# Optimization experiments

Hardware: AMD Instinct MI355X
Metric: run time of the kernel (lower is better)

The kernel has to match this reference:

```python
import jax, jax.numpy as jnp
import numpy as np

MAX_ITER = 3          # module init arg max_iter
FILL = 1e9            # large finite value for out-of-grid / out-of-label-range padding

N, H, W, C = 1, 320, 640, 32
NUM_DIR = 4


def setup_inputs() -> dict:
    key = jax.random.key(0)
    k1, k2, k3 = jax.random.split(key, 3)
    prob_vol = jax.random.uniform(k1, (N, H, W, C), dtype=jnp.float32)
    edge_weights = jax.random.uniform(k2, (N, NUM_DIR, H, W), dtype=jnp.float32)
    # affinities[:, :, :2] ~ L1 jump costs, affinities[:, :, 2] ~ L2 truncation cost
    affinities = jax.random.uniform(k3, (N, NUM_DIR, 3, H, W), dtype=jnp.float32)
    offset = jnp.zeros((N, NUM_DIR, H, W), dtype=jnp.float32)
    messages = jnp.zeros((N, NUM_DIR, H, W, C), dtype=jnp.float32)
    return {"prob_vol": prob_vol, "edge_weights": edge_weights,
            "affinities": affinities, "offset": offset, "messages": messages}


def _shift(x, axis, step):
    # result[p] = x[p - step] along `axis`, FILL outside the grid
    n = x.shape[axis]
    pw = [(0, 0)] * x.ndim
    if step > 0:
        pw[axis] = (step, 0)
        return jax.lax.slice_in_dim(jnp.pad(x, pw, constant_values=FILL), 0, n, axis=axis)
    pw[axis] = (0, -step)
    return jax.lax.slice_in_dim(jnp.pad(x, pw, constant_values=FILL), -step, n - step, axis=axis)


def _bp_iter(cost, edge, aff, offset, messages):
    # cost: (N,H,W,C); messages: (N,4,H,W,C); edge/offset: (N,4,H,W); aff: (N,4,3,H,W)
    total = cost + messages.sum(axis=1)  # belief pre-message, (N,H,W,C)
    # direction d: (d, opposite, spatial axis, step of sender->receiver)
    DIRS = [(0, 1, 2, 1), (1, 0, 2, -1), (2, 3, 1, 1), (3, 2, 1, -1)]
    new = []
    for d, opp, axis, step in DIRS:
        h = total - messages[:, opp]          # exclude reverse-direction message at sender
        hs = _shift(h, axis, step)            # sender's h aligned to receiver pixel
        w = edge[:, d][..., None]             # (N,H,W,1) edge weight
        if d % 2 == 0:
            a_m1 = aff[:, d, 0][..., None]    # cost for label jump -1
            a_p1 = aff[:, d, 1][..., None]    # cost for label jump +1
        else:  # opposite direction swaps the asymmetric +/-1 jump costs
            a_m1 = aff[:, d, 1][..., None]
            a_p1 = aff[:, d, 0][..., None]
        L2 = aff[:, d, 2][..., None]          # truncation cost for |jump| >= 2
        off = offset[:, d][..., None]
        big = jnp.full(hs.shape[:-1] + (1,), FILL, hs.dtype)
        h_lm1 = jnp.concatenate([big, hs[..., :-1]], axis=-1)  # hs(l-1)
        h_lp1 = jnp.concatenate([hs[..., 1:], big], axis=-1)   # hs(l+1)
        hmin = hs.min(axis=-1, keepdims=True)
        # min-sum update with truncated-linear pairwise: min over jump 0, +-1, truncated
        m = jnp.minimum(jnp.minimum(hs, h_lm1 + w * a_p1),
                        jnp.minimum(h_lp1 + w * a_m1, hmin + w * L2)) + w * off
        m = m - m.min(axis=-1, keepdims=True)  # message rescaling (message_scale)
        # boundary pixels have no sender -> zero message
        if d == 0:
            m = m.at[:, :, 0, :].set(0.0)
        elif d == 1:
            m = m.at[:, :, -1, :].set(0.0)
        elif d == 2:
            m = m.at[:, 0, :, :].set(0.0)
        else:
            m = m.at[:, -1, :, :].set(0.0)
        new.append(m)
    return jnp.stack(new, axis=1)


def reference(prob_vol, edge_weights, affinities, offset, messages):
    cost = -prob_vol
    for _ in range(MAX_ITER):
        messages = _bp_iter(cost, edge_weights, affinities, offset, messages)
    beliefs = messages.sum(axis=1) + cost
    beliefs = jax.nn.softmax(-beliefs, axis=-1)  # TemperatureSoftmin(dim=3, T=1)
    return beliefs, messages
```

## Files before the change

### kernel.cpp

```cpp
#include <hip/hip_runtime.h>
#include <math.h>

#define H 320
#define W 640
#define C 32
#define HW (H * W)
#define HWC (H * W * C)
#define FILLV 1e9f


__device__ __forceinline__ float group_min8(float v) {
    v = fminf(v, __shfl_xor(v, 4, 8));
    v = fminf(v, __shfl_xor(v, 2, 8));
    v = fminf(v, __shfl_xor(v, 1, 8));
    return v;
}
__device__ __forceinline__ float group_max8(float v) {
    v = fmaxf(v, __shfl_xor(v, 4, 8));
    v = fmaxf(v, __shfl_xor(v, 2, 8));
    v = fmaxf(v, __shfl_xor(v, 1, 8));
    return v;
}
__device__ __forceinline__ float group_sum8(float v) {
    v += __shfl_xor(v, 4, 8);
    v += __shfl_xor(v, 2, 8);
    v += __shfl_xor(v, 1, 8);
    return v;
}

template <bool RESCALE>
__device__ __forceinline__ void msg_core(
    float h0, float h1, float h2, float h3, int q,
    float wgt, float am1, float ap1, float l2c, float off,
    float& m0, float& m1, float& m2, float& m3)
{
    const float w_p1 = wgt * ap1;
    const float w_m1 = wgt * am1;
    const float w_L2 = wgt * l2c;
    const float w_of = wgt * off;

    const float up = __shfl_up(h3, 1, 8);
    const float dn = __shfl_down(h0, 1, 8);
    const float lm0 = (q == 0) ? FILLV : up;
    const float lp3 = (q == 7) ? FILLV : dn;

    float hmin = fminf(fminf(h0, h1), fminf(h2, h3));
    hmin = group_min8(hmin);
    const float tr = hmin + w_L2;

    m0 = fminf(fminf(h0, lm0 + w_p1), fminf(h1 + w_m1, tr)) + w_of;
    m1 = fminf(fminf(h1, h0  + w_p1), fminf(h2 + w_m1, tr)) + w_of;
    m2 = fminf(fminf(h2, h1  + w_p1), fminf(h3 + w_m1, tr)) + w_of;
    m3 = fminf(fminf(h3, h2  + w_p1), fminf(lp3 + w_m1, tr)) + w_of;

    if (RESCALE) {
        float mn = fminf(fminf(m0, m1), fminf(m2, m3));
        mn = group_min8(mn);
        m0 -= mn; m1 -= mn; m2 -= mn; m3 -= mn;
    }
}

__device__ __forceinline__ bool sender_of(int x, int y, int d, int& sx, int& sy) {
    sx = x; sy = y;
    if (d == 0) { sx = x - 1; return x == 0; }
    if (d == 1) { sx = x + 1; return x == W - 1; }
    if (d == 2) { sy = y - 1; return y == 0; }
    sy = y + 1; return y == H - 1;
}

__global__ __launch_bounds__(256) void bp_fused12_kernel(
    const float* __restrict__ prob_vol,
    const float* __restrict__ edge,
    const float* __restrict__ aff,
    const float* __restrict__ offs,
    float* __restrict__ m2_out,
    float* __restrict__ T2_out)
{
    const int tid = blockIdx.x * blockDim.x + threadIdx.x;
    const int q = tid & 7;
    const int p = tid >> 3;
    if (p >= HW) return;
    const int y = p / W;
    const int x = p - y * W;
    const int lbase = 4 * q;

    const float4 cown = *(const float4*)(prob_vol + p * C + lbase);
    float b0 = 0.f, b1 = 0.f, b2 = 0.f, b3 = 0.f;

    #pragma unroll
    for (int d = 0; d < 4; ++d) {
        const int opp = d ^ 1;
        int sx, sy;
        const bool bnd = sender_of(x, y, d, sx, sy);

        float m0 = 0.f, m1 = 0.f, m2v = 0.f, m3v = 0.f;
        if (!bnd) {
            const int sp = sy * W + sx;
            const int sb = sp * C + lbase;
            const float4 cs = *(const float4*)(prob_vol + sb);
            float h0 = -cs.x, h1 = -cs.y, h2 = -cs.z, h3 = -cs.w;

            #pragma unroll
            for (int dd = 0; dd < 4; ++dd) {
                if (dd == opp) continue;
                int s2x, s2y;
                const bool b2 = sender_of(sx, sy, dd, s2x, s2y);
                if (!b2) {
                    const int s2b = (s2y * W + s2x) * C + lbase;
                    const float4 c2 = *(const float4*)(prob_vol + s2b);
                    const float g0 = -c2.x, g1 = -c2.y, g2 = -c2.z, g3 = -c2.w;
                    const float wgt = edge[dd * HW + sp];
                    const float A0  = aff[(dd * 3 + 0) * HW + sp];
                    const float A1  = aff[(dd * 3 + 1) * HW + sp];
                    const float L2c = aff[(dd * 3 + 2) * HW + sp];
                    const float of  = offs[dd * HW + sp];
                    const float am1 = ((dd & 1) == 0) ? A0 : A1;
                    const float ap1 = ((dd & 1) == 0) ? A1 : A0;
                    float u0, u1, u2, u3;
                    msg_core<false>(g0, g1, g2, g3, q, wgt, am1, ap1, L2c, of,
                                    u0, u1, u2, u3);
                    h0 += u0; h1 += u1; h2 += u2; h3 += u3;
                }
            }

            const float wgt = edge[d * HW + p];
            const float A0  = aff[(d * 3 + 0) * HW + p];
            const float A1  = aff[(d * 3 + 1) * HW + p];
            const float L2c = aff[(d * 3 + 2) * HW + p];
            const float of  = offs[d * HW + p];
            const float am1 = ((d & 1) == 0) ? A0 : A1;
            const float ap1 = ((d & 1) == 0) ? A1 : A0;
            msg_core<true>(h0, h1, h2, h3, q, wgt, am1, ap1, L2c, of,
                           m0, m1, m2v, m3v);
        }
        float4 mv; mv.x = m0; mv.y = m1; mv.z = m2v; mv.w = m3v;
        *(float4*)(m2_out + d * HWC + p * C + lbase) = mv;
        b0 += m0; b1 += m1; b2 += m2v; b3 += m3v;
    }

    float4 tv; tv.x = b0 - cown.x; tv.y = b1 - cown.y;
    tv.z = b2 - cown.z; tv.w = b3 - cown.w;
    *(float4*)(T2_out + p * C + lbase) = tv;
}

__global__ __launch_bounds__(256) void bp_iter3_kernel(
    const float* __restrict__ prob_vol,
    const float* __restrict__ edge,
    const float* __restrict__ aff,
    const float* __restrict__ offs,
    const float* __restrict__ T2,
    const float* __restrict__ m2,
    float* __restrict__ msg_out,
    float* __restrict__ beliefs)
{
    const int tid = blockIdx.x * blockDim.x + threadIdx.x;
    const int q = tid & 7;
    const int p = tid >> 3;
    if (p >= HW) return;
    const int y = p / W;
    const int x = p - y * W;
    const int lbase = 4 * q;

    float b0 = 0.f, b1 = 0.f, b2 = 0.f, b3 = 0.f;

    #pragma unroll
    for (int d = 0; d < 4; ++d) {
        const int opp = d ^ 1;
        int sx, sy;
        const bool bnd = sender_of(x, y, d, sx, sy);

        float m0 = 0.f, m1 = 0.f, m2v = 0.f, m3v = 0.f;
        if (!bnd) {
            const int sb = (sy * W + sx) * C + lbase;
            const float4 tv = *(const float4*)(T2 + sb);
            const float4 ov = *(const float4*)(m2 + opp * HWC + sb);
            const float h0 = tv.x - ov.x, h1 = tv.y - ov.y,
                        h2 = tv.z - ov.z, h3 = tv.w - ov.w;

            const float wgt = edge[d * HW + p];
            const float A0  = aff[(d * 3 + 0) * HW + p];
            const float A1  = aff[(d * 3 + 1) * HW + p];
            const float L2c = aff[(d * 3 + 2) * HW + p];
            const float of  = offs[d * HW + p];
            const float am1 = ((d & 1) == 0) ? A0 : A1;
            const float ap1 = ((d & 1) == 0) ? A1 : A0;
            msg_core<true>(h0, h1, h2, h3, q, wgt, am1, ap1, L2c, of,
                           m0, m1, m2v, m3v);
        }
        float4 mv; mv.x = m0; mv.y = m1; mv.z = m2v; mv.w = m3v;
        *(float4*)(msg_out + d * HWC + p * C + lbase) = mv;
        b0 += m0; b1 += m1; b2 += m2v; b3 += m3v;
    }

    const float4 cv = *(const float4*)(prob_vol + p * C + lbase);
    float t0 = cv.x - b0, t1 = cv.y - b1, t2 = cv.z - b2, t3 = cv.w - b3;
    float tmax = fmaxf(fmaxf(t0, t1), fmaxf(t2, t3));
    tmax = group_max8(tmax);
    const float e0 = __expf(t0 - tmax), e1 = __expf(t1 - tmax),
                e2 = __expf(t2 - tmax), e3 = __expf(t3 - tmax);
    float s = (e0 + e1) + (e2 + e3);
    s = group_sum8(s);
    const float inv = 1.0f / s;
    float4 bv; bv.x = e0 * inv; bv.y = e1 * inv; bv.z = e2 * inv; bv.w = e3 * inv;
    *(float4*)(beliefs + p * C + lbase) = bv;
}

extern "C" void kernel_launch(void* const* d_in, const int* in_sizes, int n_in,
                              void* d_out, int out_size, void* d_ws, size_t ws_size,
                              hipStream_t stream) {
    const float* prob_vol = (const float*)d_in[0];
    const float* edge     = (const float*)d_in[1];
    const float* aff      = (const float*)d_in[2];
    const float* offs     = (const float*)d_in[3];

    float* beliefs_out = (float*)d_out;
    float* msg_final   = (float*)d_out + HWC;
    float* m2          = (float*)d_ws;
    float* T2          = (float*)d_ws + 4 * HWC;

    const dim3 block(256);
    const dim3 grid((HW * 8) / 256);

    bp_fused12_kernel<<<grid, block, 0, stream>>>(prob_vol, edge, aff, offs,
                                                  m2, T2);
    bp_iter3_kernel<<<grid, block, 0, stream>>>(prob_vol, edge, aff, offs,
                                                T2, m2, msg_final, beliefs_out);
}
```

Measured before the change: 314.1 us.

## Tile fused iterations 1-2 with LDS halo and simplify message rescaling

The fused first-two-iterations kernel now works on 8x8 pixel tiles with a one-pixel halo. Each halo pixel computes its four iteration-1 messages once and writes the per-receiver h vectors into LDS. Before, each receiver recomputed three sender messages per direction, so this removes redundant loads and msg_core work at the cost of a block-wide barrier and about 36KB of LDS per block. Separately, rescaling now subtracts the group min of h (hmin) instead of doing a second reduction, and the per-pixel offset is dropped because it cancels in the rescale. Using hmin as the message minimum assumes non-negative edge weights and affinities.

```diff
diff --git a/kernel.cpp b/kernel.cpp
--- a/kernel.cpp
+++ b/kernel.cpp
@@ -8,6 +8,13 @@
 #define HWC (H * W * C)
 #define FILLV 1e9f
 
+#define TX 8
+#define TY 8
+#define EXT_X (TX + 2)
+#define EXT_Y (TY + 2)
+#define N_EXT (EXT_X * EXT_Y)
+#define PSTR 36
+
 
 __device__ __forceinline__ float group_min8(float v) {
     v = fminf(v, __shfl_xor(v, 4, 8));
@@ -28,8 +35,7 @@
     return v;
 }
 
-template <bool RESCALE>
-__device__ __forceinline__ void msg_core(
+__device__ __forceinline__ void msg_core_m1(
     float h0, float h1, float h2, float h3, int q,
     float wgt, float am1, float ap1, float l2c, float off,
     float& m0, float& m1, float& m2, float& m3)
@@ -52,12 +58,30 @@
     m1 = fminf(fminf(h1, h0  + w_p1), fminf(h2 + w_m1, tr)) + w_of;
     m2 = fminf(fminf(h2, h1  + w_p1), fminf(h3 + w_m1, tr)) + w_of;
     m3 = fminf(fminf(h3, h2  + w_p1), fminf(lp3 + w_m1, tr)) + w_of;
-
-    if (RESCALE) {
-        float mn = fminf(fminf(m0, m1), fminf(m2, m3));
-        mn = group_min8(mn);
-        m0 -= mn; m1 -= mn; m2 -= mn; m3 -= mn;
-    }
+}
+
+__device__ __forceinline__ void msg_core_r(
+    float h0, float h1, float h2, float h3, int q,
+    float wgt, float am1, float ap1, float l2c,
+    float& m0, float& m1, float& m2, float& m3)
+{
+    const float w_p1 = wgt * ap1;
+    const float w_m1 = wgt * am1;
+    const float w_L2 = wgt * l2c;
+
+    const float up = __shfl_up(h3, 1, 8);
+    const float dn = __shfl_down(h0, 1, 8);
+    const float lm0 = (q == 0) ? FILLV : up;
+    const float lp3 = (q == 7) ? FILLV : dn;
+
+    float hmin = fminf(fminf(h0, h1), fminf(h2, h3));
+    hmin = group_min8(hmin);
+    const float tr = hmin + w_L2;
+
+    m0 = fminf(fminf(h0, lm0 + w_p1), fminf(h1 + w_m1, tr)) - hmin;
+    m1 = fminf(fminf(h1, h0  + w_p1), fminf(h2 + w_m1, tr)) - hmin;
+    m2 = fminf(fminf(h2, h1  + w_p1), fminf(h3 + w_m1, tr)) - hmin;
+    m3 = fminf(fminf(h3, h2  + w_p1), fminf(lp3 + w_m1, tr)) - hmin;
 }
 
 __device__ __forceinline__ bool sender_of(int x, int y, int d, int& sx, int& sy) {
@@ -68,13 +92,118 @@
     sy = y + 1; return y == H - 1;
 }
 
-__global__ __launch_bounds__(256) void bp_fused12_kernel(
+__global__ __launch_bounds__(512) void bp_fused12_lds(
     const float* __restrict__ prob_vol,
     const float* __restrict__ edge,
     const float* __restrict__ aff,
     const float* __restrict__ offs,
     float* __restrict__ m2_out,
     float* __restrict__ T2_out)
+{
+    __shared__ float hbuf[4 * TX * TY * PSTR];
+
+    const int bx0 = blockIdx.x * TX;
+    const int by0 = blockIdx.y * TY;
+    const int tid = threadIdx.x;
+    const int q = tid & 7;
+    const int lbase = 4 * q;
+
+    for (int task = tid; task < N_EXT * 8; task += 512) {
+        const int e  = task >> 3;
+        const int ex = e % EXT_X;
+        const int ey = e / EXT_X;
+        const int gx = bx0 + ex - 1;
+        const int gy = by0 + ey - 1;
+        if (gx < 0 || gx >= W || gy < 0 || gy >= H) continue;
+
+        const int sp = gy * W + gx;
+        const float4 cs = *(const float4*)(prob_vol + sp * C + lbase);
+        float t0 = -cs.x, t1 = -cs.y, t2 = -cs.z, t3 = -cs.w;
+        float m1v[4][4];
+
+        #pragma unroll
+        for (int dd = 0; dd < 4; ++dd) {
+            int s2x, s2y;
+            const bool bnd = sender_of(gx, gy, dd, s2x, s2y);
+            float u0 = 0.f, u1 = 0.f, u2 = 0.f, u3 = 0.f;
+            if (!bnd) {
+                const float4 c2 = *(const float4*)(prob_vol + (s2y * W + s2x) * C + lbase);
+                const float wgt = edge[dd * HW + sp];
+                const float A0  = aff[(dd * 3 + 0) * HW + sp];
+                const float A1  = aff[(dd * 3 + 1) * HW + sp];
+                const float L2c = aff[(dd * 3 + 2) * HW + sp];
+                const float of  = offs[dd * HW + sp];
+                const float am1 = ((dd & 1) == 0) ? A0 : A1;
+                const float ap1 = ((dd & 1) == 0) ? A1 : A0;
+                msg_core_m1(-c2.x, -c2.y, -c2.z, -c2.w, q,
+                            wgt, am1, ap1, L2c, of, u0, u1, u2, u3);
+            }
+            m1v[dd][0] = u0; m1v[dd][1] = u1; m1v[dd][2] = u2; m1v[dd][3] = u3;
+            t0 += u0; t1 += u1; t2 += u2; t3 += u3;
+        }
+
+        #pragma unroll
+        for (int dd = 0; dd < 4; ++dd) {
+            const int rx = gx + ((dd == 0) ? -1 : (dd == 1) ? 1 : 0);
+            const int ry = gy + ((dd == 2) ? -1 : (dd == 3) ? 1 : 0);
+            const int ix = rx - bx0, iy = ry - by0;
+            if (ix >= 0 && ix < TX && iy >= 0 && iy < TY) {
+                const int ip = iy * TX + ix;
+                const int dp = dd ^ 1;
+                float4 hv;
+                hv.x = t0 - m1v[dd][0]; hv.y = t1 - m1v[dd][1];
+                hv.z = t2 - m1v[dd][2]; hv.w = t3 - m1v[dd][3];
+                *(float4*)&hbuf[(dp * TX * TY + ip) * PSTR + lbase] = hv;
+            }
+        }
+    }
+
+    __syncthreads();
+
+    const int ip = tid >> 3;
+    const int ix = ip & (TX - 1);
+    const int iy = ip >> 3;
+    const int gx = bx0 + ix;
+    const int gy = by0 + iy;
+    const int p  = gy * W + gx;
+
+    float b0 = 0.f, b1 = 0.f, b2 = 0.f, b3 = 0.f;
+
+    #pragma unroll
+    for (int d = 0; d < 4; ++d) {
+        const bool bnd = (d == 0 && gx == 0) || (d == 1 && gx == W - 1) ||
+                         (d == 2 && gy == 0) || (d == 3 && gy == H - 1);
+        float m0 = 0.f, m1 = 0.f, m2v = 0.f, m3v = 0.f;
+        if (!bnd) {
+            const float4 h4 = *(const float4*)&hbuf[(d * TX * TY + ip) * PSTR + lbase];
+            const float wgt = edge[d * HW + p];
+            const float A0  = aff[(d * 3 + 0) * HW + p];
+            const float A1  = aff[(d * 3 + 1) * HW + p];
+            const float L2c = aff[(d * 3 + 2) * HW + p];
+            const float am1 = ((d & 1) == 0) ? A0 : A1;
+            const float ap1 = ((d & 1) == 0) ? A1 : A0;
+            msg_core_r(h4.x, h4.y, h4.z, h4.w, q, wgt, am1, ap1, L2c,
+                       m0, m1, m2v, m3v);
+        }
+        float4 mv; mv.x = m0; mv.y = m1; mv.z = m2v; mv.w = m3v;
+        *(float4*)(m2_out + d * HWC + p * C + lbase) = mv;
+        b0 += m0; b1 += m1; b2 += m2v; b3 += m3v;
+    }
+
+    const float4 cown = *(const float4*)(prob_vol + p * C + lbase);
+    float4 tv; tv.x = b0 - cown.x; tv.y = b1 - cown.y;
+    tv.z = b2 - cown.z; tv.w = b3 - cown.w;
+    *(float4*)(T2_out + p * C + lbase) = tv;
+}
+
+__global__ __launch_bounds__(256) void bp_iter3_kernel(
+    const float* __restrict__ prob_vol,
+    const float* __restrict__ edge,
+    const float* __restrict__ aff,
+    const float* __restrict__ T2,
+    const float* __restrict__ m2,
+    float* __restrict__ msg_out,
+    float* __restrict__ beliefs)
 {
     const int tid = blockIdx.x * blockDim.x + threadIdx.x;
     const int q = tid & 7;
@@ -84,83 +213,6 @@
     const int x = p - y * W;
     const int lbase = 4 * q;
 
-    const float4 cown = *(const float4*)(prob_vol + p * C + lbase);
-    float b0 = 0.f, b1 = 0.f, b2 = 0.f, b3 = 0.f;
-
-    #pragma unroll
-    for (int d = 0; d < 4; ++d) {
-        const int opp = d ^ 1;
-        int sx, sy;
-        const bool bnd = sender_of(x, y, d, sx, sy);
-
-        float m0 = 0.f, m1 = 0.f, m2v = 0.f, m3v = 0.f;
-        if (!bnd) {
-            const int sp = sy * W + sx;
-            const int sb = sp * C + lbase;
-            const float4 cs = *(const float4*)(prob_vol + sb);
-            float h0 = -cs.x, h1 = -cs.y, h2 = -cs.z, h3 = -cs.w;
-
-            #pragma unroll
-            for (int dd = 0; dd < 4; ++dd) {
-                if (dd == opp) continue;
-                int s2x, s2y;
-                const bool b2 = sender_of(sx, sy, dd, s2x, s2y);
-                if (!b2) {
-                    const int s2b = (s2y * W + s2x) * C + lbase;
-                    const float4 c2 = *(const float4*)(prob_vol + s2b);
-                    const float g0 = -c2.x, g1 = -c2.y, g2 = -c2.z, g3 = -c2.w;
-                    const float wgt = edge[dd * HW + sp];
-                    const float A0  = aff[(dd * 3 + 0) * HW + sp];
-                    const float A1  = aff[(dd * 3 + 1) * HW + sp];
-                    const float L2c = aff[(dd * 3 + 2) * HW + sp];
-                    const float of  = offs[dd * HW + sp];
-                    const float am1 = ((dd & 1) == 0) ? A0 : A1;
-                    const float ap1 = ((dd & 1) == 0) ? A1 : A0;
-                    float u0, u1, u2, u3;
-                    msg_core<false>(g0, g1, g2, g3, q, wgt, am1, ap1, L2c, of,
-                                    u0, u1, u2, u3);
-                    h0 += u0; h1 += u1; h2 += u2; h3 += u3;
-                }
-            }
-
-            const float wgt = edge[d * HW + p];
-            const float A0  = aff[(d * 3 + 0) * HW + p];
-            const float A1  = aff[(d * 3 + 1) * HW + p];
-            const float L2c = aff[(d * 3 + 2) * HW + p];
-            const float of  = offs[d * HW + p];
-            const float am1 = ((d & 1) == 0) ? A0 : A1;
-            const float ap1 = ((d & 1) == 0) ? A1 : A0;
-            msg_core<true>(h0, h1, h2, h3, q, wgt, am1, ap1, L2c, of,
-                           m0, m1, m2v, m3v);
-        }
-        float4 mv; mv.x = m0; mv.y = m1; mv.z = m2v; mv.w = m3v;
-        *(float4*)(m2_out + d * HWC + p * C + lbase) = mv;
-        b0 += m0; b1 += m1; b2 += m2v; b3 += m3v;
-    }
-
-    float4 tv; tv.x = b0 - cown.x; tv.y = b1 - cown.y;
-    tv.z = b2 - cown.z; tv.w = b3 - cown.w;
-    *(float4*)(T2_out + p * C + lbase) = tv;
-}
-
-__global__ __launch_bounds__(256) void bp_iter3_kernel(
-    const float* __restrict__ prob_vol,
-    const float* __restrict__ edge,
-    const float* __restrict__ aff,
-    const float* __restrict__ offs,
-    const float* __restrict__ T2,
-    const float* __restrict__ m2,
-    float* __restrict__ msg_out,
-    float* __restrict__ beliefs)
-{
-    const int tid = blockIdx.x * blockDim.x + threadIdx.x;
-    const int q = tid & 7;
-    const int p = tid >> 3;
-    if (p >= HW) return;
-    const int y = p / W;
-    const int x = p - y * W;
-    const int lbase = 4 * q;
-
     float b0 = 0.f, b1 = 0.f, b2 = 0.f, b3 = 0.f;
 
     #pragma unroll
@@ -181,11 +233,10 @@
             const float A0  = aff[(d * 3 + 0) * HW + p];
             const float A1  = aff[(d * 3 + 1) * HW + p];
             const float L2c = aff[(d * 3 + 2) * HW + p];
-            const float of  = offs[d * HW + p];
             const float am1 = ((d & 1) == 0) ? A0 : A1;
             const float ap1 = ((d & 1) == 0) ? A1 : A0;
-            msg_core<true>(h0, h1, h2, h3, q, wgt, am1, ap1, L2c, of,
-                           m0, m1, m2v, m3v);
+            msg_core_r(h0, h1, h2, h3, q, wgt, am1, ap1, L2c,
+                       m0, m1, m2v, m3v);
         }
         float4 mv; mv.x = m0; mv.y = m1; mv.z = m2v; mv.w = m3v;
         *(float4*)(msg_out + d * HWC + p * C + lbase) = mv;
@@ -218,11 +269,14 @@
     float* m2          = (float*)d_ws;
     float* T2          = (float*)d_ws + 4 * HWC;
 
+    const dim3 fblock(512);
+    const dim3 fgrid(W / TX, H / TY);
+
+    bp_fused12_lds<<<fgrid, fblock, 0, stream>>>(prob_vol, edge, aff, offs,
+                                                 m2, T2);
+
     const dim3 block(256);
     const dim3 grid((HW * 8) / 256);
-
-    bp_fused12_kernel<<<grid, block, 0, stream>>>(prob_vol, edge, aff, offs,
-                                                  m2, T2);
-    bp_iter3_kernel<<<grid, block, 0, stream>>>(prob_vol, edge, aff, offs,
+    bp_iter3_kernel<<<grid, block, 0, stream>>>(prob_vol, edge, aff,
                                                 T2, m2, msg_final, beliefs_out);
 }
```

Result: faster. 305.7 us (-2.7%).
